# Performance work log

Measured on AMD Instinct MI355X. Metric: run time of the kernel, lower is better.

## Reference

```python
import jax, jax.numpy as jnp
import numpy as np

GAMMA = 1.0
INPUT_DIM = 512
NUM_CENTERS = 4096
BATCH = 16384


def setup_inputs() -> dict:
    key = jax.random.key(0)
    kx, kc = jax.random.split(key)
    x = jax.random.normal(kx, (BATCH, INPUT_DIM), dtype=jnp.float32)
    centers = jax.random.normal(kc, (NUM_CENTERS, INPUT_DIM), dtype=jnp.float32)
    return {"x": x, "centers": centers}


def reference(x, centers):
    x_sq = jnp.sum(x * x, axis=-1, keepdims=True)            # [B, 1]
    c_sq = jnp.sum(centers * centers, axis=-1)               # [C]
    cross = jnp.einsum("bd,cd->bc", x, centers)              # [B, C]
    dist_sq = x_sq - 2.0 * cross + c_sq[None, :]
    return jnp.exp(-GAMMA * dist_sq)
```

## Files before the change

### kernel.cpp

```cpp
#include <hip/hip_runtime.h>
#include <stdint.h>

#define M_DIM 16384
#define N_DIM 4096
#define K_DIM 512

typedef int v8i __attribute__((ext_vector_type(8)));
typedef float f32x16 __attribute__((ext_vector_type(16)));
typedef float f32x4v __attribute__((ext_vector_type(4)));

typedef __attribute__((address_space(3))) uint32_t lds_u32_t;
typedef const __attribute__((address_space(1))) uint32_t glob_u32_t;

__device__ __forceinline__ void gload16(const void* g, void* l) {
    __builtin_amdgcn_global_load_lds((glob_u32_t*)g, (lds_u32_t*)l, 16, 0, 0);
}

__global__ __launch_bounds__(256)
void convert_norm_kernel(const float* __restrict__ X, const float* __restrict__ C,
                         uint8_t* __restrict__ Apack, uint8_t* __restrict__ Bf8,
                         float* __restrict__ xsq, float* __restrict__ csq) {
    const int bid = blockIdx.x;
    const int t = threadIdx.x;

    if (bid < 512) {
        __shared__ float sums[4][32];
        const int P = bid;
        const int r = (t >> 1) & 31;
        const int w = t >> 6;
        const float* Xs = X + (size_t)P * 32 * K_DIM;
        uint8_t* dst = Apack + (size_t)P * 16384;
        float s = 0.f;
        #pragma unroll
        for (int i = 0; i < 4; ++i) {
            const int q = i * 256 + t;
            const int c0 = (q >> 7) * 64 + ((q >> 6) & 1) * 32 + (q & 1) * 16;
            const float4* p = (const float4*)(Xs + (size_t)r * K_DIM + c0);
            float4 f0 = p[0], f1 = p[1], f2 = p[2], f3 = p[3];
            uint32_t d0 = 0, d1 = 0, d2 = 0, d3 = 0;
            d0 = __builtin_amdgcn_cvt_pk_fp8_f32(f0.x, f0.y, d0, false);
            d0 = __builtin_amdgcn_cvt_pk_fp8_f32(f0.z, f0.w, d0, true);
            d1 = __builtin_amdgcn_cvt_pk_fp8_f32(f1.x, f1.y, d1, false);
            d1 = __builtin_amdgcn_cvt_pk_fp8_f32(f1.z, f1.w, d1, true);
            d2 = __builtin_amdgcn_cvt_pk_fp8_f32(f2.x, f2.y, d2, false);
            d2 = __builtin_amdgcn_cvt_pk_fp8_f32(f2.z, f2.w, d2, true);
            d3 = __builtin_amdgcn_cvt_pk_fp8_f32(f3.x, f3.y, d3, false);
            d3 = __builtin_amdgcn_cvt_pk_fp8_f32(f3.z, f3.w, d3, true);
            *(uint4*)(dst + (size_t)q * 16) = make_uint4(d0, d1, d2, d3);
            s += f0.x*f0.x + f0.y*f0.y + f0.z*f0.z + f0.w*f0.w
               + f1.x*f1.x + f1.y*f1.y + f1.z*f1.z + f1.w*f1.w
               + f2.x*f2.x + f2.y*f2.y + f2.z*f2.z + f2.w*f2.w
               + f3.x*f3.x + f3.y*f3.y + f3.z*f3.z + f3.w*f3.w;
        }
        s += __shfl_xor(s, 1, 64);
        if ((t & 1) == 0) sums[w][r] = s;
        __syncthreads();
        if (t < 32)
            xsq[P * 32 + t] = sums[0][t] + sums[1][t] + sums[2][t] + sums[3][t];
    } else {
        const int wave = t >> 6;
        const int lane = t & 63;
        const int rr = (bid - 512) * 4 + wave;
        const float4* p = (const float4*)(C + (size_t)rr * K_DIM) + lane * 2;
        float4 a = p[0], b = p[1];
        uint32_t lo = 0, hi = 0;
        lo = __builtin_amdgcn_cvt_pk_fp8_f32(a.x, a.y, lo, false);
        lo = __builtin_amdgcn_cvt_pk_fp8_f32(a.z, a.w, lo, true);
        hi = __builtin_amdgcn_cvt_pk_fp8_f32(b.x, b.y, hi, false);
        hi = __builtin_amdgcn_cvt_pk_fp8_f32(b.z, b.w, hi, true);
        *(uint2*)(Bf8 + (size_t)rr * K_DIM + lane * 8) = make_uint2(lo, hi);

        float s = a.x*a.x + a.y*a.y + a.z*a.z + a.w*a.w
                + b.x*b.x + b.y*b.y + b.z*b.z + b.w*b.w;
        #pragma unroll
        for (int o2 = 32; o2 > 0; o2 >>= 1) s += __shfl_down(s, o2, 64);
        if (lane == 0) csq[rr] = s;
    }
}

__global__ __launch_bounds__(256, 4)
void rbf_mfma_kernel(const uint8_t* __restrict__ Apack, const uint8_t* __restrict__ B8,
                     const float* __restrict__ xsq, const float* __restrict__ csq,
                     float* __restrict__ out) {
    __shared__ uint8_t Bs[128 * 128];

    const int tid = threadIdx.x;
    const int lv  = tid & 63;
    const int w   = tid >> 6;
    const int h   = lv >> 5;
    const int r31 = lv & 31;

    const int bn = (blockIdx.x & 31) * 128;
    const int bm = (blockIdx.x >> 5) * 128;

    const int tr = tid >> 3;
    const int tc = tid & 7;
    const int cc = (tc - tr) & 7;
    const uint8_t* gB = B8 + (size_t)(bn + 4 * tr) * K_DIM + cc * 16;
    uint8_t* BsW = Bs + w * 1024;

    const uint8_t* aB = Apack + (size_t)((bm >> 5) + w) * 16384 + h * 1024 + r31 * 32;

    const uint8_t* bRow = Bs + r31 * 128;

    f32x16 acc[4] = {};

    for (int kk = 0; kk < 4; ++kk) {
        const int koff = kk * 128;
        #pragma unroll
        for (int R = 0; R < 4; ++R)
            gload16(gB + koff + (size_t)R * K_DIM, BsW + R * 4096);

        uint4 a0[2], a1[2];
        #pragma unroll
        for (int ksl = 0; ksl < 2; ++ksl) {
            const uint8_t* ap = aB + (2 * kk + ksl) * 2048;
            a0[ksl] = *(const uint4*)(ap);
            a1[ksl] = *(const uint4*)(ap + 16);
        }
        __syncthreads();

        #pragma unroll
        for (int ksl = 0; ksl < 2; ++ksl) {
            v8i av = (v8i){(int)a0[ksl].x, (int)a0[ksl].y, (int)a0[ksl].z, (int)a0[ksl].w,
                           (int)a1[ksl].x, (int)a1[ksl].y, (int)a1[ksl].z, (int)a1[ksl].w};
            const int c0 = ksl * 4 + 2 * h;
            const int s0 = ((c0 + 0 + r31) & 7) * 16;
            const int s1 = ((c0 + 1 + r31) & 7) * 16;
            #pragma unroll
            for (int j = 0; j < 4; ++j) {
                uint4 lo = *(const uint4*)(bRow + j * 4096 + s0);
                uint4 hi = *(const uint4*)(bRow + j * 4096 + s1);
                v8i bv = (v8i){(int)lo.x, (int)lo.y, (int)lo.z, (int)lo.w,
                               (int)hi.x, (int)hi.y, (int)hi.z, (int)hi.w};
                acc[j] = __builtin_amdgcn_mfma_scale_f32_32x32x64_f8f6f4(
                    av, bv, acc[j],
                    0 , 0 ,
                    0, 0x7F7F7F7Fu, 0, 0x7F7F7F7Fu);
            }
        }
        if (kk < 3) __syncthreads();
    }

    const float4 cs4 = *(const float4*)(csq + bn + 4 * r31);
    const int mbase = bm + 32 * w + 4 * h;

    #pragma unroll
    for (int g = 0; g < 4; ++g) {
        const float4 xs4 = *(const float4*)(xsq + mbase + 8 * g);
        #pragma unroll
        for (int rr = 0; rr < 4; ++rr) {
            const int reg = g * 4 + rr;
            const float xs = (rr == 0) ? xs4.x : (rr == 1) ? xs4.y
                           : (rr == 2) ? xs4.z : xs4.w;
            const int gm = mbase + 8 * g + rr;
            f32x4v o;
            o.x = __expf(-(xs - 2.0f * acc[0][reg] + cs4.x));
            o.y = __expf(-(xs - 2.0f * acc[1][reg] + cs4.y));
            o.z = __expf(-(xs - 2.0f * acc[2][reg] + cs4.z));
            o.w = __expf(-(xs - 2.0f * acc[3][reg] + cs4.w));
            __builtin_nontemporal_store(
                o, (f32x4v*)(out + (size_t)gm * N_DIM + bn + 4 * r31));
        }
    }
}

extern "C" void kernel_launch(void* const* d_in, const int* in_sizes, int n_in,
                              void* d_out, int out_size, void* d_ws, size_t ws_size,
                              hipStream_t stream) {
    const float* X = (const float*)d_in[0];
    const float* C = (const float*)d_in[1];
    float* out = (float*)d_out;

    uint8_t* Apack = (uint8_t*)d_ws;
    uint8_t* Bf8 = Apack + (size_t)M_DIM * K_DIM;
    float* xsq = (float*)(Bf8 + (size_t)N_DIM * K_DIM);
    float* csq = xsq + M_DIM;

    convert_norm_kernel<<<512 + N_DIM / 4, 256, 0, stream>>>(X, C, Apack, Bf8, xsq, csq);
    rbf_mfma_kernel<<<(M_DIM / 128) * (N_DIM / 128), 256, 0, stream>>>(Apack, Bf8, xsq, csq, out);
}
```

Before: 300.4 us.

## Stage full K of B tile in LDS upfront and preload all A fragments

```diff
diff --git a/kernel.cpp b/kernel.cpp
--- a/kernel.cpp
+++ b/kernel.cpp
@@ -78,11 +78,11 @@
     }
 }
 
-__global__ __launch_bounds__(256, 4)
+__global__ __launch_bounds__(256, 2)
 void rbf_mfma_kernel(const uint8_t* __restrict__ Apack, const uint8_t* __restrict__ B8,
                      const float* __restrict__ xsq, const float* __restrict__ csq,
                      float* __restrict__ out) {
-    __shared__ uint8_t Bs[128 * 128];
+    __shared__ uint8_t Bs[4 * 128 * 128];
 
     const int tid = threadIdx.x;
     const int lv  = tid & 63;
@@ -99,38 +99,48 @@
     const uint8_t* gB = B8 + (size_t)(bn + 4 * tr) * K_DIM + cc * 16;
     uint8_t* BsW = Bs + w * 1024;
 
+    #pragma unroll
+    for (int kk = 0; kk < 4; ++kk)
+        #pragma unroll
+        for (int R = 0; R < 4; ++R)
+            gload16(gB + kk * 128 + (size_t)R * K_DIM, BsW + kk * 16384 + R * 4096);
+
     const uint8_t* aB = Apack + (size_t)((bm >> 5) + w) * 16384 + h * 1024 + r31 * 32;
+    uint4 a0[8], a1[8];
+    #pragma unroll
+    for (int ks = 0; ks < 8; ++ks) {
+        const uint8_t* ap = aB + ks * 2048;
+        a0[ks] = *(const uint4*)(ap);
+        a1[ks] = *(const uint4*)(ap + 16);
+    }
+
+    const float4 cs4 = *(const float4*)(csq + bn + 4 * r31);
+    const int mbase = bm + 32 * w + 4 * h;
+    float4 xs4[4];
+    #pragma unroll
+    for (int g = 0; g < 4; ++g)
+        xs4[g] = *(const float4*)(xsq + mbase + 8 * g);
+
+    __syncthreads();
 
     const uint8_t* bRow = Bs + r31 * 128;
-
     f32x16 acc[4] = {};
 
+    #pragma unroll
     for (int kk = 0; kk < 4; ++kk) {
-        const int koff = kk * 128;
-        #pragma unroll
-        for (int R = 0; R < 4; ++R)
-            gload16(gB + koff + (size_t)R * K_DIM, BsW + R * 4096);
-
-        uint4 a0[2], a1[2];
         #pragma unroll
         for (int ksl = 0; ksl < 2; ++ksl) {
-            const uint8_t* ap = aB + (2 * kk + ksl) * 2048;
-            a0[ksl] = *(const uint4*)(ap);
-            a1[ksl] = *(const uint4*)(ap + 16);
-        }
-        __syncthreads();
-
-        #pragma unroll
-        for (int ksl = 0; ksl < 2; ++ksl) {
-            v8i av = (v8i){(int)a0[ksl].x, (int)a0[ksl].y, (int)a0[ksl].z, (int)a0[ksl].w,
-                           (int)a1[ksl].x, (int)a1[ksl].y, (int)a1[ksl].z, (int)a1[ksl].w};
+            const int ks = 2 * kk + ksl;
+            v8i av = (v8i){(int)a0[ks].x, (int)a0[ks].y, (int)a0[ks].z, (int)a0[ks].w,
+                           (int)a1[ks].x, (int)a1[ks].y, (int)a1[ks].z, (int)a1[ks].w};
             const int c0 = ksl * 4 + 2 * h;
             const int s0 = ((c0 + 0 + r31) & 7) * 16;
             const int s1 = ((c0 + 1 + r31) & 7) * 16;
             #pragma unroll
             for (int j = 0; j < 4; ++j) {
-                uint4 lo = *(const uint4*)(bRow + j * 4096 + s0);
-                uint4 hi = *(const uint4*)(bRow + j * 4096 + s1);
+                const uint8_t* seg = bRow + kk * 16384 + j * 4096;
+                uint4 lo = *(const uint4*)(seg + s0);
+                uint4 hi = *(const uint4*)(seg + s1);
                 v8i bv = (v8i){(int)lo.x, (int)lo.y, (int)lo.z, (int)lo.w,
                                (int)hi.x, (int)hi.y, (int)hi.z, (int)hi.w};
                 acc[j] = __builtin_amdgcn_mfma_scale_f32_32x32x64_f8f6f4(
@@ -139,20 +149,15 @@
                     0, 0x7F7F7F7Fu, 0, 0x7F7F7F7Fu);
             }
         }
-        if (kk < 3) __syncthreads();
     }
-
-    const float4 cs4 = *(const float4*)(csq + bn + 4 * r31);
-    const int mbase = bm + 32 * w + 4 * h;
 
     #pragma unroll
     for (int g = 0; g < 4; ++g) {
-        const float4 xs4 = *(const float4*)(xsq + mbase + 8 * g);
         #pragma unroll
         for (int rr = 0; rr < 4; ++rr) {
             const int reg = g * 4 + rr;
-            const float xs = (rr == 0) ? xs4.x : (rr == 1) ? xs4.y
-                           : (rr == 2) ? xs4.z : xs4.w;
+            const float xs = (rr == 0) ? xs4[g].x : (rr == 1) ? xs4[g].y
+                           : (rr == 2) ? xs4[g].z : xs4[g].w;
             const int gm = mbase + 8 * g + rr;
             f32x4v o;
             o.x = __expf(-(xs - 2.0f * acc[0][reg] + cs4.x));
```

Result: no change. 302.8 us (+0.8%).
